# Optimization experiments

Hardware: AMD Instinct MI355X
Metric: run time of the kernel (lower is better)

The kernel has to match this reference:

```python
import jax, jax.numpy as jnp
import numpy as np
from jax import lax


def build_perm_matrix(C, num_filters):
    """Replicates the nested-loop combinatorial channel-group sums in Net.permconv
    as a static [G, C] 0/1 coefficient matrix (G = num_perm groups)."""
    ncpf = C // num_filters  # num_channels_per_filter
    G = num_filters + ncpf * ((num_filters - 1) * num_filters) // 2
    M = np.zeros((G, C), dtype=np.float32)
    count = 0
    for i in range(num_filters):
        for j in range(ncpf):
            if j == 0:
                for k in range(i, num_filters):
                    M[count, i * ncpf + j] += 1.0
                    M[count, k * ncpf + 1:k * ncpf + ncpf] += 1.0
                    count += 1
            else:
                for k in range(i + 1, num_filters):
                    M[count, i * ncpf + j] += 1.0
                    M[count, k * ncpf:k * ncpf + j] += 1.0
                    M[count, k * ncpf + j + 1:k * ncpf + ncpf] += 1.0
                    count += 1
    assert count == G
    return M


# Static index maps (stage 1: 30ch/10 filters -> 145 groups; stage 2: 600ch/6 filters -> 1506 groups)
_M1 = jnp.asarray(build_perm_matrix(30, 10))
_M2 = jnp.asarray(build_perm_matrix(600, 6))


def _dwconv(x, w, b, groups):
    y = lax.conv_general_dilated(x, w, window_strides=(1, 1), padding=[(1, 1), (1, 1)],
                                 feature_group_count=groups,
                                 dimension_numbers=('NCHW', 'OIHW', 'NCHW'))
    return y + b[None, :, None, None]


def _permconv(x, dw_w, dw_b, pw_w, pw_b, M, groups):
    y = _dwconv(x, dw_w, dw_b, groups)            # [B, C, H, W]
    g = jnp.einsum('gc,bchw->bghw', M, y)         # combinatorial group sums
    g = jax.nn.relu(g)
    return jnp.einsum('og,bghw->bohw', pw_w, g) + pw_b[None, :, None, None]  # 1x1 conv


def _maxpool2(x):
    return lax.reduce_window(x, -jnp.inf, lax.max, (1, 1, 2, 2), (1, 1, 2, 2), 'VALID')


def setup_inputs() -> dict:
    key = jax.random.key(0)
    ks = jax.random.split(key, 13)
    p = lambda k, s: (jax.random.normal(k, s, jnp.float32) * 0.05)
    return {
        'x': jax.random.normal(ks[0], (500, 3, 32, 32), jnp.float32),
        'dw1_w': p(ks[1], (30, 1, 3, 3)),  'dw1_b': p(ks[2], (30,)),
        'pw1_w': p(ks[3], (100, 145)),     'pw1_b': p(ks[4], (100,)),
        'dw2_w': p(ks[5], (600, 1, 3, 3)), 'dw2_b': p(ks[6], (600,)),
        'pw2_w': p(ks[7], (300, 1506)),    'pw2_b': p(ks[8], (300,)),
        'fc1_w': p(ks[9], (120, 19200)),   'fc1_b': p(ks[10], (120,)),
        'fc2_w': p(ks[11], (10, 120)),     'fc2_b': p(ks[12], (10,)),
    }


def reference(x, dw1_w, dw1_b, pw1_w, pw1_b, dw2_w, dw2_b, pw2_w, pw2_b,
              fc1_w, fc1_b, fc2_w, fc2_b):
    h = _permconv(x, dw1_w, dw1_b, pw1_w, pw1_b, _M1, groups=3)    # [500,100,32,32]
    h = _maxpool2(jax.nn.relu(h))                                  # [500,100,16,16]
    h = _permconv(h, dw2_w, dw2_b, pw2_w, pw2_b, _M2, groups=100)  # [500,300,16,16]
    h = _maxpool2(jax.nn.relu(h))                                  # [500,300,8,8]
    h = h.reshape(h.shape[0], -1)                                  # [500,19200] (NCHW flatten)
    h = h @ fc1_w.T + fc1_b
    return h @ fc2_w.T + fc2_b                                     # [500,10]
```

## Files before the change

kernel.cpp:

```cpp
#include <hip/hip_runtime.h>

#define NF1 10
#define NCPF1 3
#define G1 145
#define G2 1506
#define KTOT 1536
#define NKT2 48
#define NS 20

typedef __attribute__((ext_vector_type(8))) short bf16x8;
typedef __attribute__((ext_vector_type(4))) float f32x4;

__device__ __forceinline__ ushort rne_bf16(float v) {
  union { float f; uint u; } a; a.f = v;
  return (ushort)((a.u + 0x7fffu + ((a.u >> 16) & 1u)) >> 16);
}
__device__ __forceinline__ float bf_to_f(ushort s) {
  union { uint u; float f; } a; a.u = ((uint)s) << 16;
  return a.f;
}
__device__ __forceinline__ void bsplit(float v, ushort& h, ushort& l) {
  union { float f; uint u; } a; a.f = v;
  uint hu = (a.u + 0x7fffu + ((a.u >> 16) & 1u)) >> 16;
  union { uint u; float f; } hf; hf.u = hu << 16;
  union { float f; uint u; } b2; b2.f = v - hf.f;
  h = (ushort)hu;
  l = (ushort)((b2.u + 0x7fffu + ((b2.u >> 16) & 1u)) >> 16);
}

__device__ __forceinline__ void barrier_lds() {
  asm volatile("s_waitcnt lgkmcnt(0)" ::: "memory");
  __builtin_amdgcn_s_barrier();
}

__global__ void build_tables1(int* __restrict__ piv1, int* __restrict__ kk1, int* __restrict__ kj1) {
  int t = threadIdx.x;
  if (t < NF1) {
    int i = t;
    int base = 0;
    for (int ii = 0; ii < i; ++ii) base += (NF1 - ii) + (NCPF1 - 1) * (NF1 - 1 - ii);
    int count = base;
    for (int j = 0; j < NCPF1; ++j) {
      int k0 = (j == 0) ? i : (i + 1);
      for (int k = k0; k < NF1; ++k) {
        piv1[count] = i * NCPF1 + j;
        kk1[count] = k;
        kj1[count] = k * NCPF1 + j;
        ++count;
      }
    }
  }
}

__global__ void build_perm2(int* __restrict__ gmap, ushort* __restrict__ gPkS, uint* __restrict__ ktsC) {
  int t = threadIdx.x;
  if (t >= NKT2) return;
  int chans[NS];
  int nch = 0;
  int pivs[32], kjs[32];
  int base = t * 32;
  for (int u = 0; u < 32; ++u) {
    int g = base + u;
    if (g >= G2) { pivs[u] = -1; kjs[u] = -1; gmap[g] = -1; gPkS[g] = 0; continue; }
    int i, j, k;
    if (g < 21) {
      j = 0; int r = g; i = 0; int len = 6;
      while (r >= len) { r -= len; ++i; len = 6 - i; }
      k = i + r;
    } else {
      int gp = g - 21; j = 1 + gp / 15; int r = gp % 15; i = 0; int len = 5;
      while (r >= len) { r -= len; ++i; len = 5 - i; }
      k = i + 1 + r;
    }
    pivs[u] = i * 100 + j; kjs[u] = k * 100 + j;
    int ob = (i == 0) ? 0 : (i == 1) ? 501 : (i == 2) ? 902 : (i == 3) ? 1203 : (i == 4) ? 1404 : 1505;
    int old;
    if (j == 0) old = ob + (k - i);
    else old = ob + (6 - i) + (j - 1) * (5 - i) + (k - i - 1);
    gmap[g] = old;
  }
  for (int u = 0; u < 32; ++u) {
    int g = base + u;
    if (g >= G2) continue;
    int ps = -1, ks2 = -1;
    for (int q = 0; q < nch; ++q) {
      if (chans[q] == pivs[u]) ps = q;
      if (chans[q] == kjs[u]) ks2 = q;
    }
    if (ps < 0) { ps = nch; chans[nch++] = pivs[u]; }
    if (ks2 < 0) { ks2 = nch; chans[nch++] = kjs[u]; }
    int f = kjs[u] / 100;
    gPkS[g] = (ushort)(ps | (ks2 << 5) | (f << 10));
  }
  for (int q = 0; q < NS; ++q) {
    int ch = (q < nch) ? chans[q] : 0;
    ktsC[t * NS + q] = (uint)ch | ((uint)(ch / 6) << 10);
  }
}

__global__ __launch_bounds__(256) void prep_w2(const float* __restrict__ pw2w, const int* __restrict__ gmap,
                                               ushort* __restrict__ whi) {
  int idx = blockIdx.x * 256 + threadIdx.x;
  if (idx >= 320 * KTOT) return;
  int oc = idx / KTOT, k = idx % KTOT;
  int old = gmap[k];
  float v = (oc < 300 && old >= 0) ? pw2w[oc * G2 + old] : 0.f;
  whi[idx] = rne_bf16(v);
}

__global__ __launch_bounds__(256) void prep_w1(const float* __restrict__ pw1w, ushort* __restrict__ p1h,
                                               ushort* __restrict__ p1l) {
  int idx = blockIdx.x * 256 + threadIdx.x;
  if (idx >= 128 * 160) return;
  int oc = idx / 160, k = idx % 160;
  float v = (oc < 100 && k < G1) ? pw1w[oc * G1 + k] : 0.f;
  ushort h, l;
  bsplit(v, h, l);
  p1h[idx] = h;
  p1l[idx] = l;
}

__global__ __launch_bounds__(256) void prep_dw2(const float* __restrict__ dw2w, const float* __restrict__ dw2b,
                                                float* __restrict__ dw2p) {
  int c = blockIdx.x * 256 + threadIdx.x;
  if (c >= 600) return;
  for (int q = 0; q < 9; ++q) dw2p[c * 12 + q] = dw2w[c * 9 + q];
  dw2p[c * 12 + 9] = dw2b[c];
  dw2p[c * 12 + 10] = 0.f;
  dw2p[c * 12 + 11] = 0.f;
}

__global__ void prep_wcomb(const float* __restrict__ dw2w, const float* __restrict__ dw2b,
                           float* __restrict__ wcomb, float* __restrict__ bcomb) {
  int idx = threadIdx.x + blockIdx.x * 256;
  if (idx < 6 * 18 * 9) {
    int f = idx / 162, s = (idx % 162) / 9, tap = idx % 9;
    int ic = (f * 100) / 6 + s;
    int clo = f * 100, chi = f * 100 + 100;
    int ilo = ic * 6, ihi = ic * 6 + 6;
    int lo = clo > ilo ? clo : ilo;
    int hi = chi < ihi ? chi : ihi;
    float sacc = 0.f;
    for (int c = lo; c < hi; ++c) sacc += dw2w[c * 9 + tap];
    wcomb[idx] = sacc;
  }
  if (idx < 6) {
    float sacc = 0.f;
    for (int m = 0; m < 100; ++m) sacc += dw2b[idx * 100 + m];
    bcomb[idx] = sacc;
  }
}

__global__ __launch_bounds__(256) void stage1f(const float* __restrict__ x, const float* __restrict__ dw1w,
                                               const float* __restrict__ dw1b, const ushort* __restrict__ p1h,
                                               const ushort* __restrict__ p1l, const float* __restrict__ pw1b,
                                               const int* __restrict__ piv, const int* __restrict__ kk,
                                               const int* __restrict__ kj, ushort* __restrict__ h1) {
  __shared__ float xs[3][4][34];
  __shared__ float ys[30][64];
  __shared__ float Ss[NF1][64];
  __shared__ ushort g[64][168];
  __shared__ uint tbl[G1];

  int b = blockIdx.x >> 4;
  int oh = blockIdx.x & 15;
  int t = threadIdx.x;
  int lane = t & 63, wave = t >> 6;
  int lrow = lane & 15, lkk = lane >> 4;

  if (t < G1) tbl[t] = (uint)piv[t] | ((uint)kj[t] << 8) | ((uint)kk[t] << 16);
  for (int idx = t; idx < 3 * 4 * 34; idx += 256) {
    int c = idx / 136, rem = idx % 136;
    int r = rem / 34, cc = rem % 34;
    int row = 2 * oh - 1 + r, col = cc - 1;
    float v = 0.f;
    if (row >= 0 && row < 32 && col >= 0 && col < 32) v = x[(((size_t)b * 3 + c) * 32 + row) * 32 + col];
    xs[c][r][cc] = v;
  }
  __syncthreads();
  for (int idx = t; idx < 30 * 64; idx += 256) {
    int c = idx >> 6, p = idx & 63;
    int rr = p >> 5, w = p & 31;
    int ic = c / 10;
    float acc = dw1b[c];
#pragma unroll
    for (int kh = 0; kh < 3; ++kh)
#pragma unroll
      for (int kw = 0; kw < 3; ++kw) acc += xs[ic][rr + kh][w + kw] * dw1w[c * 9 + kh * 3 + kw];
    ys[c][p] = acc;
  }
  __syncthreads();
  for (int idx = t; idx < NF1 * 64; idx += 256) {
    int f = idx >> 6, p = idx & 63;
    Ss[f][p] = ys[3 * f][p] + ys[3 * f + 1][p] + ys[3 * f + 2][p];
  }
  __syncthreads();
  {
    int n = t >> 2, qd = t & 3;
    int sub = n >> 4, ow = n & 15;
    int px = 32 * (sub >> 1) + 2 * ow + (sub & 1);
#pragma unroll
    for (int pass = 0; pass < 10; ++pass) {
      int k0 = pass * 16 + qd * 4;
      union { ushort us[4]; unsigned long long v; } pv;
#pragma unroll
      for (int c = 0; c < 4; ++c) {
        int k = k0 + c;
        float val = 0.f;
        if (k < G1) {
          uint tb = tbl[k];
          val = fmaxf(ys[(tb & 255)][px] + Ss[(tb >> 16)][px] - ys[((tb >> 8) & 255)][px], 0.f);
        }
        pv.us[c] = rne_bf16(val);
      }
      *(unsigned long long*)&g[n][k0] = pv.v;
    }
  }
  __syncthreads();
  f32x4 acc[2][4];
#pragma unroll
  for (int mt = 0; mt < 2; ++mt)
#pragma unroll
    for (int nt = 0; nt < 4; ++nt) acc[mt][nt] = (f32x4){0.f, 0.f, 0.f, 0.f};
#pragma unroll
  for (int ks = 0; ks < 5; ++ks) {
    int koff = ks * 32 + lkk * 8;
    bf16x8 Bh[4];
#pragma unroll
    for (int nt = 0; nt < 4; ++nt) Bh[nt] = *(const bf16x8*)&g[nt * 16 + lrow][koff];
#pragma unroll
    for (int mt = 0; mt < 2; ++mt) {
      int row = wave * 32 + mt * 16 + lrow;
      bf16x8 Ah = *(const bf16x8*)(p1h + row * 160 + koff);
      bf16x8 Al = *(const bf16x8*)(p1l + row * 160 + koff);
#pragma unroll
      for (int nt = 0; nt < 4; ++nt) {
        f32x4 c = acc[mt][nt];
        c = __builtin_amdgcn_mfma_f32_16x16x32_bf16(Ah, Bh[nt], c, 0, 0, 0);
        c = __builtin_amdgcn_mfma_f32_16x16x32_bf16(Al, Bh[nt], c, 0, 0, 0);
        acc[mt][nt] = c;
      }
    }
  }
#pragma unroll
  for (int mt = 0; mt < 2; ++mt) {
#pragma unroll
    for (int r = 0; r < 4; ++r) {
      int oc = wave * 32 + mt * 16 + lkk * 4 + r;
      if (oc < 100) {
        float v = fmaxf(fmaxf(acc[mt][0][r], acc[mt][1][r]), fmaxf(acc[mt][2][r], acc[mt][3][r]));
        float h = fmaxf(v + pw1b[oc], 0.f);
        h1[((size_t)b * 100 + oc) * 256 + oh * 16 + lrow] = rne_bf16(h);
      }
    }
  }
}

__global__ __launch_bounds__(512, 4) void stage2f(
    const ushort* __restrict__ h1, const ushort* __restrict__ whi,
    const float* __restrict__ dw2p, const float* __restrict__ wcomb, const float* __restrict__ bcomb,
    const float* __restrict__ pw2b, const ushort* __restrict__ gPkS, const uint* __restrict__ ktsC,
    ushort* __restrict__ h2) {
  __shared__ ushort h1s[100][6][18];
  __shared__ float y2c[2][NS][72];
  __shared__ ushort Gh[2][64][40];
  __shared__ float Slp[6][72];
  __shared__ ushort gPk[KTOT];
  __shared__ uint kts[NKT2 * NS];

  int blk = blockIdx.x;
  int b = blk >> 2, q = blk & 3;
  int t = threadIdx.x;
  int lane = t & 63, wave = t >> 6;
  int lrow = lane & 15, lkk = lane >> 4;

  for (int i = t; i < KTOT / 2; i += 512) ((uint*)gPk)[i] = ((const uint*)gPkS)[i];
  for (int i = t; i < NKT2 * NS; i += 512) kts[i] = ktsC[i];
  for (int i = t; i < 5400; i += 512) ((uint*)h1s)[i] = 0u;
  __syncthreads();
  const ushort* hb = h1 + (size_t)b * 25600;
  for (int i = t; i < 600; i += 512) {
    int ic = i / 6, rr = i % 6;
    int hr = 4 * q - 1 + rr;
    if (hr >= 0 && hr < 16) {
      const ushort* src = hb + ic * 256 + hr * 16;
      ushort* dst = &h1s[ic][rr][1];
#pragma unroll
      for (int c2 = 0; c2 < 16; ++c2) dst[c2] = src[c2];
    }
  }
  __syncthreads();
  for (int i = t; i < 6 * 64; i += 512) {
    int f = i >> 6, p = i & 63;
    int r = p >> 4, w = p & 15;
    int iclo = (f * 100) / 6;
    float s = bcomb[f];
    for (int ss2 = 0; ss2 < 18; ++ss2) {
      int ic = iclo + ss2;
      if (ic > 99) ic = 99;
      const float* wv = wcomb + (f * 18 + ss2) * 9;
#pragma unroll
      for (int dh = 0; dh < 3; ++dh)
#pragma unroll
        for (int dw = 0; dw < 3; ++dw) s += wv[dh * 3 + dw] * bf_to_f(h1s[ic][r + dh][w + dw]);
    }
    Slp[f][p] = s;
  }
  __syncthreads();

  if (wave < 4) {
    int n = t & 63;
    int koct = wave;
    bool doC1 = (t < 160);
    int slot = t >> 3, r = (t >> 1) & 3, half = t & 1;
    uint ktN = 0;
    float4 waN = {0, 0, 0, 0}, wbN = {0, 0, 0, 0}, wcN = {0, 0, 0, 0};
    if (doC1) {
      ktN = kts[slot];
      const float4* wp4 = (const float4*)(dw2p + (ktN & 1023) * 12);
      waN = wp4[0]; wbN = wp4[1]; wcN = wp4[2];
    }
    uint4 pkN = {0, 0, 0, 0};
    for (int s = 0; s <= NKT2 + 1; ++s) {
      uint ktC = ktN;
      float4 waC = waN, wbC = wbN, wcC = wcN;
      uint4 pkC = pkN;
      if (s < NKT2) pkN = *(const uint4*)&gPk[s * 32 + koct * 8];
      if (doC1 && s + 1 < NKT2) {
        ktN = kts[(s + 1) * NS + slot];
        const float4* wp4 = (const float4*)(dw2p + (ktN & 1023) * 12);
        waN = wp4[0]; wbN = wp4[1]; wcN = wp4[2];
      }
      if (s >= 1 && s <= NKT2) {
        int bc = (s - 1) & 1;
        union { ushort us[8]; bf16x8 v; } ph;
        uint pks[4] = {pkC.x, pkC.y, pkC.z, pkC.w};
#pragma unroll
        for (int c = 0; c < 8; ++c) {
          uint pk = (pks[c >> 1] >> ((c & 1) * 16)) & 0xffffu;
          int ps = pk & 31, ks = (pk >> 5) & 31, f = (pk >> 10) & 7;
          float v = fmaxf(y2c[bc][ps][n] + Slp[f][n] - y2c[bc][ks][n], 0.f);
          ph.us[c] = rne_bf16(v);
        }
        uint off = (uint)bc * 5120u + (uint)n * 80u + (uint)((koct ^ (n & 3)) * 16);
        *(bf16x8*)((char*)Gh + off) = ph.v;
      }
      if (s < NKT2 && doC1) {
        int ic = (ktC >> 10) & 127;
        int w0 = half * 8;
        float fr[3][10];
#pragma unroll
        for (int dr = 0; dr < 3; ++dr)
#pragma unroll
          for (int cc = 0; cc < 10; ++cc) fr[dr][cc] = bf_to_f(h1s[ic][r + dr][w0 + cc]);
        float* dst = &y2c[s & 1][slot][r * 16 + w0];
#pragma unroll
        for (int w = 0; w < 8; ++w) {
          float sa = wcC.y;
          sa += fr[0][w] * waC.x + fr[0][w + 1] * waC.y + fr[0][w + 2] * waC.z;
          sa += fr[1][w] * waC.w + fr[1][w + 1] * wbC.x + fr[1][w + 2] * wbC.y;
          sa += fr[2][w] * wbC.z + fr[2][w + 1] * wbC.w + fr[2][w + 2] * wcC.x;
          dst[w] = sa;
        }
      }
      barrier_lds();
    }
  } else {
    int cw = wave - 4;
    f32x4 acc[5][4];
#pragma unroll
    for (int mt = 0; mt < 5; ++mt)
#pragma unroll
      for (int nt = 0; nt < 4; ++nt) acc[mt][nt] = (f32x4){0.f, 0.f, 0.f, 0.f};
    bf16x8 Ah[5];

    for (int s = 0; s <= NKT2 + 1; ++s) {
      int km = s - 2;
      if (km >= 0) {
        int bm = km & 1;
        const char* gb = (const char*)Gh + bm * 5120;
        __builtin_amdgcn_s_setprio(1);
#pragma unroll
        for (int half = 0; half < 2; ++half) {
          bf16x8 B0, B1;
          {
            int n0 = (half * 2) * 16 + lrow, n1 = (half * 2 + 1) * 16 + lrow;
            B0 = *(const bf16x8*)(gb + (uint)n0 * 80u + (uint)((lkk ^ (n0 & 3)) * 16));
            B1 = *(const bf16x8*)(gb + (uint)n1 * 80u + (uint)((lkk ^ (n1 & 3)) * 16));
          }
#pragma unroll
          for (int mt = 0; mt < 5; ++mt) {
            acc[mt][half * 2] =
                __builtin_amdgcn_mfma_f32_16x16x32_bf16(Ah[mt], B0, acc[mt][half * 2], 0, 0, 0);
            acc[mt][half * 2 + 1] =
                __builtin_amdgcn_mfma_f32_16x16x32_bf16(Ah[mt], B1, acc[mt][half * 2 + 1], 0, 0, 0);
          }
        }
        __builtin_amdgcn_s_setprio(0);
      }
      int ka = s - 1;
      if (ka >= 0 && ka < NKT2) {
        const size_t wof = (size_t)(cw * 80 + lrow) * KTOT + (size_t)ka * 32 + (size_t)lkk * 8;
#pragma unroll
        for (int mt = 0; mt < 5; ++mt)
          Ah[mt] = *(const bf16x8*)(whi + wof + (size_t)mt * 16 * KTOT);
      }
      barrier_lds();
    }

#pragma unroll
    for (int mt = 0; mt < 5; ++mt) {
      int ocb = cw * 80 + mt * 16 + lkk * 4;
#pragma unroll
      for (int r = 0; r < 4; ++r) {
        float v01 = fmaxf(acc[mt][0][r], acc[mt][1][r]);
        float v23 = fmaxf(acc[mt][2][r], acc[mt][3][r]);
        v01 = fmaxf(v01, __shfl_xor(v01, 1));
        v23 = fmaxf(v23, __shfl_xor(v23, 1));
        int oc = ocb + r;
        if ((lane & 1) == 0 && oc < 300) {
          float b0 = pw2b[oc];
          size_t base = ((size_t)b * 300 + oc) * 64;
          h2[base + (q * 2 + 0) * 8 + (lrow >> 1)] = rne_bf16(fmaxf(v01 + b0, 0.f));
          h2[base + (q * 2 + 1) * 8 + (lrow >> 1)] = rne_bf16(fmaxf(v23 + b0, 0.f));
        }
      }
    }
  }
}

__global__ __launch_bounds__(256) void fold_fc(const float* __restrict__ fc1w, const float* __restrict__ fc2w,
                                               float* __restrict__ combW) {
  int idx = blockIdx.x * 256 + threadIdx.x;
  if (idx >= 10 * 19200) return;
  int o = idx / 19200, c = idx % 19200;
  float s = 0.f;
  for (int m = 0; m < 120; ++m) s += fc2w[o * 120 + m] * fc1w[m * 19200 + c];
  combW[idx] = s;
}

__global__ void fold_b(const float* __restrict__ fc1b, const float* __restrict__ fc2w,
                       const float* __restrict__ fc2b, float* __restrict__ combB) {
  int o = threadIdx.x;
  if (o < 10) {
    float s = fc2b[o];
    for (int m = 0; m < 120; ++m) s += fc2w[o * 120 + m] * fc1b[m];
    combB[o] = s;
  }
}

__global__ __launch_bounds__(256) void fc_out(const ushort* __restrict__ h2, const float* __restrict__ combW,
                                              const float* __restrict__ combB, float* __restrict__ out, int b0) {
  int b = blockIdx.x / 10, o = blockIdx.x % 10;
  const ushort* hp = h2 + (size_t)b * 19200;
  const float* wp = combW + (size_t)o * 19200;
  float s = 0.f;
  for (int idx = threadIdx.x; idx < 2400; idx += 256) {
    bf16x8 hv = *(const bf16x8*)(hp + idx * 8);
    float4 w0 = *(const float4*)(wp + idx * 8);
    float4 w1 = *(const float4*)(wp + idx * 8 + 4);
    s += bf_to_f((ushort)hv[0]) * w0.x + bf_to_f((ushort)hv[1]) * w0.y;
    s += bf_to_f((ushort)hv[2]) * w0.z + bf_to_f((ushort)hv[3]) * w0.w;
    s += bf_to_f((ushort)hv[4]) * w1.x + bf_to_f((ushort)hv[5]) * w1.y;
    s += bf_to_f((ushort)hv[6]) * w1.z + bf_to_f((ushort)hv[7]) * w1.w;
  }
  __shared__ float red[256];
  red[threadIdx.x] = s;
  __syncthreads();
  for (int stride = 128; stride > 0; stride >>= 1) {
    if (threadIdx.x < stride) red[threadIdx.x] += red[threadIdx.x + stride];
    __syncthreads();
  }
  if (threadIdx.x == 0) out[(size_t)(b0 + b) * 10 + o] = red[0] + combB[o];
}

extern "C" void kernel_launch(void* const* d_in, const int* in_sizes, int n_in,
                              void* d_out, int out_size, void* d_ws, size_t ws_size,
                              hipStream_t stream) {
  const float* x = (const float*)d_in[0];
  const float* dw1w = (const float*)d_in[1];
  const float* dw1b = (const float*)d_in[2];
  const float* pw1w = (const float*)d_in[3];
  const float* pw1b = (const float*)d_in[4];
  const float* dw2w = (const float*)d_in[5];
  const float* dw2b = (const float*)d_in[6];
  const float* pw2w = (const float*)d_in[7];
  const float* pw2b = (const float*)d_in[8];
  const float* fc1w = (const float*)d_in[9];
  const float* fc1b = (const float*)d_in[10];
  const float* fc2w = (const float*)d_in[11];
  const float* fc2b = (const float*)d_in[12];
  float* out = (float*)d_out;

  char* ws = (char*)d_ws;
  size_t off = 0;
  auto alloc = [&](size_t bytes) -> void* {
    off = (off + 255) & ~(size_t)255;
    void* p = ws + off;
    off += bytes;
    return p;
  };
  int* piv1 = (int*)alloc(G1 * 4);
  int* kk1 = (int*)alloc(G1 * 4);
  int* kj1 = (int*)alloc(G1 * 4);
  int* gmap = (int*)alloc(KTOT * 4);
  ushort* gPkS = (ushort*)alloc(KTOT * 2);
  uint* ktsC = (uint*)alloc(NKT2 * NS * 4);
  float* combW = (float*)alloc((size_t)10 * 19200 * 4);
  float* combB = (float*)alloc(16 * 4);
  ushort* whi = (ushort*)alloc((size_t)320 * KTOT * 2);
  ushort* p1h = (ushort*)alloc((size_t)128 * 160 * 2);
  ushort* p1l = (ushort*)alloc((size_t)128 * 160 * 2);
  float* dw2p = (float*)alloc((size_t)600 * 12 * 4);
  float* wcombp = (float*)alloc((size_t)6 * 18 * 9 * 4);
  float* bcombp = (float*)alloc(8 * 4);
  size_t static_end = (off + 255) & ~(size_t)255;

  size_t per_img = 51200 + 38400;
  long long avail = (long long)ws_size - (long long)static_end - 4096;
  int CB = 1;
  if (avail > 0) {
    long long c = avail / (long long)(per_img + 512);
    if (c > 500) c = 500;
    if (c < 1) c = 1;
    CB = (int)c;
  }
  ushort* h1 = (ushort*)alloc((size_t)CB * 25600 * 2);
  ushort* h2 = (ushort*)alloc((size_t)CB * 19200 * 2);

  build_tables1<<<1, 64, 0, stream>>>(piv1, kk1, kj1);
  build_perm2<<<1, 64, 0, stream>>>(gmap, gPkS, ktsC);
  prep_dw2<<<3, 256, 0, stream>>>(dw2w, dw2b, dw2p);
  prep_wcomb<<<4, 256, 0, stream>>>(dw2w, dw2b, wcombp, bcombp);
  prep_w2<<<(320 * KTOT + 255) / 256, 256, 0, stream>>>(pw2w, gmap, whi);
  prep_w1<<<(128 * 160 + 255) / 256, 256, 0, stream>>>(pw1w, p1h, p1l);
  fold_fc<<<(10 * 19200 + 255) / 256, 256, 0, stream>>>(fc1w, fc2w, combW);
  fold_b<<<1, 64, 0, stream>>>(fc1b, fc2w, fc2b, combB);

  for (int b0 = 0; b0 < 500; b0 += CB) {
    int nb = 500 - b0 < CB ? 500 - b0 : CB;
    stage1f<<<nb * 16, 256, 0, stream>>>(x + (size_t)b0 * 3 * 1024, dw1w, dw1b, p1h, p1l, pw1b,
                                         piv1, kk1, kj1, h1);
    stage2f<<<nb * 4, 512, 0, stream>>>(h1, whi, dw2p, wcombp, bcombp, pw2b,
                                        gPkS, ktsC, h2);
    fc_out<<<nb * 10, 256, 0, stream>>>(h2, combW, combB, out, b0);
  }
}
```

Baseline: 553.9 us.

## Rebalance stage2 depthwise conv work across producer waves and precompute difference buffer

The depthwise conv producer work is split into 4-pixel tasks spread over all 256 producer threads (plus an extra 64-thread pass) instead of 160 threads doing 8 pixels each. Each task also writes a second LDS buffer holding Slp minus the conv output, so the group-sum step needs only two LDS reads per element instead of three. The LDS swizzle for the Gh tile gains an extra XOR term to reduce bank conflicts. The cost is more LDS space (ddc) and an unbalanced extra pass for the first wave.

```diff
diff --git a/kernel.cpp b/kernel.cpp
--- a/kernel.cpp
+++ b/kernel.cpp
@@ -31,6 +31,10 @@
 __device__ __forceinline__ void barrier_lds() {
   asm volatile("s_waitcnt lgkmcnt(0)" ::: "memory");
   __builtin_amdgcn_s_barrier();
+}
+
+__device__ __forceinline__ uint gsw(int n, int oct) {
+  return (uint)n * 80u + (uint)(((oct ^ (n & 3) ^ ((n >> 3) & 3)) & 3) * 16);
 }
 
 __global__ void build_tables1(int* __restrict__ piv1, int* __restrict__ kk1, int* __restrict__ kj1) {
@@ -94,7 +98,7 @@
   }
   for (int q = 0; q < NS; ++q) {
     int ch = (q < nch) ? chans[q] : 0;
-    ktsC[t * NS + q] = (uint)ch | ((uint)(ch / 6) << 10);
+    ktsC[t * NS + q] = (uint)ch | ((uint)(ch / 6) << 10) | ((uint)(ch / 100) << 17);
   }
 }
 
@@ -263,6 +267,7 @@
     ushort* __restrict__ h2) {
   __shared__ ushort h1s[100][6][18];
   __shared__ float y2c[2][NS][72];
+  __shared__ float ddc[2][NS][72];
   __shared__ ushort Gh[2][64][40];
   __shared__ float Slp[6][72];
   __shared__ ushort gPk[KTOT];
@@ -311,23 +316,18 @@
   if (wave < 4) {
     int n = t & 63;
     int koct = wave;
-    bool doC1 = (t < 160);
-    int slot = t >> 3, r = (t >> 1) & 3, half = t & 1;
-    uint ktN = 0;
-    float4 waN = {0, 0, 0, 0}, wbN = {0, 0, 0, 0}, wcN = {0, 0, 0, 0};
-    if (doC1) {
-      ktN = kts[slot];
-      const float4* wp4 = (const float4*)(dw2p + (ktN & 1023) * 12);
-      waN = wp4[0]; wbN = wp4[1]; wcN = wp4[2];
-    }
+    int slot0 = t >> 4, rem0 = t & 15, r0 = rem0 >> 2, qt0 = rem0 & 3;
+    uint ktN = kts[slot0];
+    const float4* wpN = (const float4*)(dw2p + (ktN & 1023) * 12);
+    float4 waN = wpN[0], wbN = wpN[1], wcN = wpN[2];
     uint4 pkN = {0, 0, 0, 0};
     for (int s = 0; s <= NKT2 + 1; ++s) {
       uint ktC = ktN;
       float4 waC = waN, wbC = wbN, wcC = wcN;
       uint4 pkC = pkN;
       if (s < NKT2) pkN = *(const uint4*)&gPk[s * 32 + koct * 8];
-      if (doC1 && s + 1 < NKT2) {
-        ktN = kts[(s + 1) * NS + slot];
+      if (s + 1 < NKT2) {
+        ktN = kts[(s + 1) * NS + slot0];
         const float4* wp4 = (const float4*)(dw2p + (ktN & 1023) * 12);
         waN = wp4[0]; wbN = wp4[1]; wcN = wp4[2];
       }
@@ -338,29 +338,64 @@
 #pragma unroll
         for (int c = 0; c < 8; ++c) {
           uint pk = (pks[c >> 1] >> ((c & 1) * 16)) & 0xffffu;
-          int ps = pk & 31, ks = (pk >> 5) & 31, f = (pk >> 10) & 7;
-          float v = fmaxf(y2c[bc][ps][n] + Slp[f][n] - y2c[bc][ks][n], 0.f);
+          int ps = pk & 31, ks = (pk >> 5) & 31;
+          float v = fmaxf(y2c[bc][ps][n] + ddc[bc][ks][n], 0.f);
           ph.us[c] = rne_bf16(v);
         }
-        uint off = (uint)bc * 5120u + (uint)n * 80u + (uint)((koct ^ (n & 3)) * 16);
+        uint off = (uint)bc * 5120u + gsw(n, koct);
         *(bf16x8*)((char*)Gh + off) = ph.v;
       }
-      if (s < NKT2 && doC1) {
-        int ic = (ktC >> 10) & 127;
-        int w0 = half * 8;
-        float fr[3][10];
-#pragma unroll
-        for (int dr = 0; dr < 3; ++dr)
-#pragma unroll
-          for (int cc = 0; cc < 10; ++cc) fr[dr][cc] = bf_to_f(h1s[ic][r + dr][w0 + cc]);
-        float* dst = &y2c[s & 1][slot][r * 16 + w0];
-#pragma unroll
-        for (int w = 0; w < 8; ++w) {
-          float sa = wcC.y;
-          sa += fr[0][w] * waC.x + fr[0][w + 1] * waC.y + fr[0][w + 2] * waC.z;
-          sa += fr[1][w] * waC.w + fr[1][w + 1] * wbC.x + fr[1][w + 2] * wbC.y;
-          sa += fr[2][w] * wbC.z + fr[2][w + 1] * wbC.w + fr[2][w + 2] * wcC.x;
-          dst[w] = sa;
+      if (s < NKT2) {
+        {
+          int ic = (ktC >> 10) & 127, f = (int)(ktC >> 17);
+          int w0 = qt0 * 4;
+          int px = r0 * 16 + w0;
+          float fr[3][6];
+#pragma unroll
+          for (int dr = 0; dr < 3; ++dr)
+#pragma unroll
+            for (int cc = 0; cc < 6; ++cc) fr[dr][cc] = bf_to_f(h1s[ic][r0 + dr][w0 + cc]);
+          f32x4 sl = *(const f32x4*)&Slp[f][px];
+          f32x4 yv, dv;
+#pragma unroll
+          for (int w = 0; w < 4; ++w) {
+            float sa = wcC.y;
+            sa += fr[0][w] * waC.x + fr[0][w + 1] * waC.y + fr[0][w + 2] * waC.z;
+            sa += fr[1][w] * waC.w + fr[1][w + 1] * wbC.x + fr[1][w + 2] * wbC.y;
+            sa += fr[2][w] * wbC.z + fr[2][w + 1] * wbC.w + fr[2][w + 2] * wcC.x;
+            yv[w] = sa;
+            dv[w] = sl[w] - sa;
+          }
+          *(f32x4*)&y2c[s & 1][slot0][px] = yv;
+          *(f32x4*)&ddc[s & 1][slot0][px] = dv;
+        }
+        if (t < 64) {
+          int task = 256 + t;
+          int slot = task >> 4, rem = task & 15, r = rem >> 2, qt = rem & 3;
+          uint ci = kts[s * NS + slot];
+          int chan = ci & 1023, ic = (ci >> 10) & 127, f = (int)(ci >> 17);
+          const float4* wp4 = (const float4*)(dw2p + chan * 12);
+          float4 wa = wp4[0], wb4 = wp4[1], wc4 = wp4[2];
+          int w0 = qt * 4;
+          int px = r * 16 + w0;
+          float fr[3][6];
+#pragma unroll
+          for (int dr = 0; dr < 3; ++dr)
+#pragma unroll
+            for (int cc = 0; cc < 6; ++cc) fr[dr][cc] = bf_to_f(h1s[ic][r + dr][w0 + cc]);
+          f32x4 sl = *(const f32x4*)&Slp[f][px];
+          f32x4 yv, dv;
+#pragma unroll
+          for (int w = 0; w < 4; ++w) {
+            float sa = wc4.y;
+            sa += fr[0][w] * wa.x + fr[0][w + 1] * wa.y + fr[0][w + 2] * wa.z;
+            sa += fr[1][w] * wa.w + fr[1][w + 1] * wb4.x + fr[1][w + 2] * wb4.y;
+            sa += fr[2][w] * wb4.z + fr[2][w + 1] * wb4.w + fr[2][w + 2] * wc4.x;
+            yv[w] = sa;
+            dv[w] = sl[w] - sa;
+          }
+          *(f32x4*)&y2c[s & 1][slot][px] = yv;
+          *(f32x4*)&ddc[s & 1][slot][px] = dv;
         }
       }
       barrier_lds();
@@ -385,8 +420,8 @@
           bf16x8 B0, B1;
           {
             int n0 = (half * 2) * 16 + lrow, n1 = (half * 2 + 1) * 16 + lrow;
-            B0 = *(const bf16x8*)(gb + (uint)n0 * 80u + (uint)((lkk ^ (n0 & 3)) * 16));
-            B1 = *(const bf16x8*)(gb + (uint)n1 * 80u + (uint)((lkk ^ (n1 & 3)) * 16));
+            B0 = *(const bf16x8*)(gb + gsw(n0, lkk));
+            B1 = *(const bf16x8*)(gb + gsw(n1, lkk));
           }
 #pragma unroll
           for (int mt = 0; mt < 5; ++mt) {
```

New measurement: 606.6 us. 9.5% more time.
